# Kernel tuning notes

Hardware: AMD Instinct MI355X
Metric: run time of the kernel (lower is better)

The kernel has to match this reference:

```python
import jax, jax.numpy as jnp
import numpy as np

DIM = 256
NUM_HEADS = 4
FRAMES = 8
B_ = 32768
INNER = DIM // 2              # 128
HEAD_DIM = INNER // NUM_HEADS # 32 (actual per-head dim in forward)
SCALE = (DIM // NUM_HEADS) ** -0.5  # faithful: init uses dim//num_heads = 64


def _rel_pos_index():
    # window_size = [FRAMES, 1, 1] -> index depends only on temporal offset
    d = np.arange(FRAMES)
    idx = d[:, None] - d[None, :] + (FRAMES - 1)  # [N, N] in [0, 2F-2]
    return jnp.asarray(idx, dtype=jnp.int32)


def setup_inputs() -> dict:
    key = jax.random.key(0)
    ks = jax.random.split(key, 5)
    x = jax.random.normal(ks[0], (B_, FRAMES, DIM), dtype=jnp.float32)
    qkv_w = jax.random.normal(ks[1], (DIM, INNER * 3), dtype=jnp.float32) * 0.02
    proj_w = jax.random.normal(ks[2], (INNER, DIM), dtype=jnp.float32) * 0.02
    proj_b = jnp.zeros((DIM,), dtype=jnp.float32)
    bias_table = jax.random.normal(ks[3], (2 * FRAMES - 1, NUM_HEADS), dtype=jnp.float32) * 0.02
    rel_index = _rel_pos_index()
    return {"x": x, "qkv_w": qkv_w, "proj_w": proj_w, "proj_b": proj_b,
            "bias_table": bias_table, "rel_index": rel_index}


def reference(x, qkv_w, proj_w, proj_b, bias_table, rel_index):
    B, N, C = x.shape
    h, hd = NUM_HEADS, HEAD_DIM
    qkv = (x @ qkv_w).reshape(B, N, 3, h, hd)
    qkv = jnp.transpose(qkv, (2, 0, 3, 1, 4))  # [3, B, h, N, hd]
    q, k, v = qkv[0], qkv[1], qkv[2]
    attn = jnp.einsum('bhnd,bhmd->bhnm', q * SCALE, k)  # [B, h, N, N]
    # gather relative position bias: [N, N, h] -> [h, N, N]
    bias = bias_table[rel_index[:N, :N]]  # [N, N, h]
    attn = attn + jnp.transpose(bias, (2, 0, 1))[None]
    attn = jax.nn.softmax(attn, axis=-1)
    out = jnp.einsum('bhnm,bhmd->bhnd', attn, v)       # [B, h, N, hd]
    out = jnp.transpose(out, (0, 2, 1, 3)).reshape(B, N, h * hd)  # [B, N, 128]
    return out @ proj_w + proj_b
```

## Files before the change

### kernel.cpp

```cpp
#include <hip/hip_runtime.h>
#include <hip/hip_bf16.h>

typedef short bf16x8 __attribute__((ext_vector_type(8)));
typedef float f32x4 __attribute__((ext_vector_type(4)));

#define B_TOT    32768
#define ROWS     64

#define WSQ_ELT  0
#define WSP_ELT  98304
#define WS_BYTES 262144

#define WQ_OFF   0
#define QK_OFF   26112
#define BIAS_OFF 39424
#define PB_OFF   40704
#define OUT_OFF  0
#define LDS_BYTES 41728

__device__ __forceinline__ unsigned short f2b(float f) {
    union { float f; unsigned u; } v; v.f = f;
    unsigned r = (v.u + 0x7fffu + ((v.u >> 16) & 1u)) >> 16;
    return (unsigned short)r;
}
__device__ __forceinline__ float b2f(unsigned short u) {
    union { unsigned u; float f; } v; v.u = ((unsigned)u) << 16; return v.f;
}

__global__ __launch_bounds__(256)
void prep_w(const float* __restrict__ qkv_w, const float* __restrict__ proj_w,
            unsigned short* __restrict__ ws)
{
    __shared__ float tile[64][65];
    const int bid = blockIdx.x;
    const float* src; unsigned short* dst; int ldw, ldk, tr0, tc0;
    if (bid < 24) {
        int kr = bid / 6, cg = bid % 6;
        src = qkv_w; dst = ws + WSQ_ELT; ldw = 384; ldk = 256;
        tr0 = kr * 64; tc0 = cg * 64;
    } else {
        int b = bid - 24; int kr = b / 4, cg = b % 4;
        src = proj_w; dst = ws + WSP_ELT; ldw = 256; ldk = 128;
        tr0 = kr * 64; tc0 = cg * 64;
    }
    const int t = threadIdx.x;
    #pragma unroll
    for (int i = 0; i < 16; ++i) {
        int idx = i * 256 + t;
        int r = idx >> 6, c = idx & 63;
        tile[r][c] = src[(size_t)(tr0 + r) * ldw + tc0 + c];
    }
    __syncthreads();
    #pragma unroll
    for (int i = 0; i < 2; ++i) {
        int idx = i * 256 + t;
        int c = idx >> 3, r0 = (idx & 7) * 8;
        union { unsigned short u[8]; uint4 v; } pk;
        #pragma unroll
        for (int j = 0; j < 8; ++j) pk.u[j] = f2b(tile[r0 + j][c]);
        *(uint4*)&dst[(size_t)(tc0 + c) * ldk + tr0 + r0] = pk.v;
    }
}

__global__ __launch_bounds__(256)
void ta_fused(const float* __restrict__ x,
              const unsigned short* __restrict__ ws,
              const float* __restrict__ proj_b,
              const float* __restrict__ bias_table,
              const int* __restrict__ rel_index,
              float* __restrict__ out)
{
    __shared__ __align__(16) char smem[LDS_BYTES];
    unsigned short* wqs = (unsigned short*)(smem + WQ_OFF);
    unsigned short* qks = (unsigned short*)(smem + QK_OFF);
    float* bias_s = (float*)(smem + BIAS_OFF);
    float* pbs    = (float*)(smem + PB_OFF);
    float* outs   = (float*)(smem + OUT_OFF);

    const unsigned short* wsq = ws + WSQ_ELT;
    const unsigned short* wsp = ws + WSP_ELT;

    const int tid = threadIdx.x;
    const int l   = tid & 63;
    const int w   = tid >> 6;
    const int l15 = l & 15;
    const int l4  = l >> 4;
    const long wg = blockIdx.x;

    bf16x8 af[8];
    {
        const float* xg = x + wg * (ROWS * 256) + (size_t)(16 * w + l15) * 256;
        #pragma unroll
        for (int s = 0; s < 8; ++s) {
            f32x4 d0 = *(const f32x4*)(xg + s * 32 + l4 * 8);
            f32x4 d1 = *(const f32x4*)(xg + s * 32 + l4 * 8 + 4);
            union { unsigned short u[8]; bf16x8 v; } pk;
            #pragma unroll
            for (int j = 0; j < 4; ++j) pk.u[j] = f2b(d0[j]);
            #pragma unroll
            for (int j = 0; j < 4; ++j) pk.u[4 + j] = f2b(d1[j]);
            af[s] = pk.v;
        }
    }
    {
        int n = tid >> 5, m = (tid >> 2) & 7, hh = tid & 3;
        int ri = rel_index[n * 8 + m];
        bias_s[n * 40 + m * 5 + hh] = bias_table[ri * 4 + hh];
        pbs[tid] = proj_b[tid];
    }

    bf16x8 ofrag0, ofrag1, ofrag2, ofrag3;
    const f32x4 zero4 = {0.f, 0.f, 0.f, 0.f};

    #pragma unroll 1
    for (int h = 0; h < 4; ++h) {
        f32x4 acc[6];
        #pragma unroll
        for (int i = 0; i < 6; ++i) acc[i] = zero4;

        #pragma unroll
        for (int c = 0; c < 2; ++c) {
            __syncthreads();
            #pragma unroll
            for (int u = 0; u < 6; ++u) {
                int idx = u * 256 + tid;
                int rr = idx >> 4, seg = idx & 15;
                int p = rr >> 5, within = rr & 31;
                uint4 d = *(const uint4*)&wsq[(size_t)(p * 128 + h * 32 + within) * 256 + c * 128 + seg * 8];
                *(uint4*)&wqs[rr * 136 + seg * 8] = d;
            }
            __syncthreads();
            #pragma unroll
            for (int ks2 = 0; ks2 < 4; ++ks2) {
                bf16x8 a = af[c * 4 + ks2];
                #pragma unroll
                for (int ct = 0; ct < 6; ++ct) {
                    bf16x8 b = *(bf16x8*)&wqs[(ct * 16 + l15) * 136 + ks2 * 32 + l4 * 8];
                    acc[ct] = __builtin_amdgcn_mfma_f32_16x16x32_bf16(a, b, acc[ct], 0, 0, 0);
                }
            }
        }
        #pragma unroll
        for (int ct = 0; ct < 6; ++ct) {
            #pragma unroll
            for (int j = 0; j < 4; ++j) {
                int row = 16 * w + l4 * 4 + j;
                qks[row * 104 + ct * 16 + l15] = f2b(acc[ct][j]);
            }
        }
        __syncthreads();

        {
            const int r  = 16 * w + l15;
            const int rb = r & ~7;
            const int n  = r & 7;
            const int ds = l4;
            float qf[8];
            {
                bf16x8 qv = *(bf16x8*)&qks[r * 104 + ds * 8];
                #pragma unroll
                for (int j = 0; j < 8; ++j) qf[j] = b2f((unsigned short)qv[j]);
            }
            float sp[8];
            #pragma unroll
            for (int m = 0; m < 8; ++m) {
                bf16x8 kv = *(bf16x8*)&qks[(rb + m) * 104 + 32 + ds * 8];
                float s = 0.f;
                #pragma unroll
                for (int j = 0; j < 8; ++j) s += qf[j] * b2f((unsigned short)kv[j]);
                sp[m] = s;
            }
            #pragma unroll
            for (int m = 0; m < 8; ++m) {
                sp[m] += __shfl_xor(sp[m], 16);
                sp[m] += __shfl_xor(sp[m], 32);
            }
            float mx = -1e30f;
            #pragma unroll
            for (int m = 0; m < 8; ++m) {
                sp[m] = sp[m] * 0.125f + bias_s[n * 40 + m * 5 + h];
                mx = fmaxf(mx, sp[m]);
            }
            float sum = 0.f;
            #pragma unroll
            for (int m = 0; m < 8; ++m) { sp[m] = __expf(sp[m] - mx); sum += sp[m]; }
            float inv = 1.f / sum;
            float o[8] = {0.f,0.f,0.f,0.f,0.f,0.f,0.f,0.f};
            #pragma unroll
            for (int m = 0; m < 8; ++m) {
                bf16x8 vv = *(bf16x8*)&qks[(rb + m) * 104 + 64 + ds * 8];
                #pragma unroll
                for (int j = 0; j < 8; ++j) o[j] += sp[m] * b2f((unsigned short)vv[j]);
            }
            bf16x8 of;
            #pragma unroll
            for (int j = 0; j < 8; ++j) of[j] = (short)f2b(o[j] * inv);
            if      (h == 0) ofrag0 = of;
            else if (h == 1) ofrag1 = of;
            else if (h == 2) ofrag2 = of;
            else             ofrag3 = of;
        }
    }

    f32x4 acc2[16];
    #pragma unroll
    for (int i = 0; i < 16; ++i) acc2[i] = zero4;

    #pragma unroll
    for (int cc = 0; cc < 4; ++cc) {
        __syncthreads();
        #pragma unroll
        for (int u = 0; u < 4; ++u) {
            int idx = u * 256 + tid;
            int rr = idx >> 4, seg = idx & 15;
            uint4 d = *(const uint4*)&wsp[(size_t)(cc * 64 + rr) * 128 + seg * 8];
            *(uint4*)&wqs[rr * 136 + seg * 8] = d;
        }
        __syncthreads();
        #pragma unroll
        for (int ctl = 0; ctl < 4; ++ctl) {
            #pragma unroll
            for (int ks = 0; ks < 4; ++ks) {
                bf16x8 b = *(bf16x8*)&wqs[(ctl * 16 + l15) * 136 + ks * 32 + l4 * 8];
                bf16x8 a = (ks == 0) ? ofrag0 : (ks == 1) ? ofrag1 : (ks == 2) ? ofrag2 : ofrag3;
                acc2[cc * 4 + ctl] = __builtin_amdgcn_mfma_f32_16x16x32_bf16(a, b, acc2[cc * 4 + ctl], 0, 0, 0);
            }
        }
    }

    #pragma unroll
    for (int half = 0; half < 2; ++half) {
        __syncthreads();
        if ((w < 2) == (half == 0)) {
            #pragma unroll
            for (int cc = 0; cc < 4; ++cc)
              #pragma unroll
              for (int ctl = 0; ctl < 4; ++ctl)
                #pragma unroll
                for (int j = 0; j < 4; ++j) {
                    int row = 16 * (w & 1) + l4 * 4 + j;
                    int col = cc * 64 + ctl * 16 + l15;
                    outs[row * 260 + col] = acc2[cc * 4 + ctl][j] + pbs[col];
                }
        }
        __syncthreads();
        float* og = out + wg * (ROWS * 256) + half * (32 * 256);
        #pragma unroll
        for (int i = 0; i < 4; ++i) {
            int f0 = (i * 256 + tid) * 8;
            int row = f0 >> 8, col = f0 & 255;
            f32x4 v0 = *(f32x4*)&outs[row * 260 + col];
            f32x4 v1 = *(f32x4*)&outs[row * 260 + col + 4];
            *(f32x4*)(og + f0)     = v0;
            *(f32x4*)(og + f0 + 4) = v1;
        }
    }
}

extern "C" void kernel_launch(void* const* d_in, const int* in_sizes, int n_in,
                              void* d_out, int out_size, void* d_ws, size_t ws_size,
                              hipStream_t stream)
{
    (void)in_sizes; (void)n_in; (void)ws_size; (void)out_size;
    const float* x  = (const float*)d_in[0];
    const float* qw = (const float*)d_in[1];
    const float* pw = (const float*)d_in[2];
    const float* pb = (const float*)d_in[3];
    const float* bt = (const float*)d_in[4];
    const int*   ri = (const int*)d_in[5];
    float* o = (float*)d_out;
    unsigned short* ws = (unsigned short*)d_ws;

    hipLaunchKernelGGL(prep_w, dim3(32), dim3(256), 0, stream, qw, pw, ws);
    hipLaunchKernelGGL(ta_fused, dim3(B_TOT / 8), dim3(256), 0, stream,
                       x, ws, pb, bt, ri, o);
}
```

Baseline: 237.2 us.

## Double rows per workgroup so each wave reuses staged weight tiles across two M-tiles

```diff
diff --git a/kernel.cpp b/kernel.cpp
--- a/kernel.cpp
+++ b/kernel.cpp
@@ -4,24 +4,22 @@
 typedef short bf16x8 __attribute__((ext_vector_type(8)));
 typedef float f32x4 __attribute__((ext_vector_type(4)));
 
-#define B_TOT    32768
-#define ROWS     64
+#define B_TOT 32768
+#define ROWS  128
 
 #define WSQ_ELT  0
 #define WSP_ELT  98304
-#define WS_BYTES 262144
 
 #define WQ_OFF   0
 #define QK_OFF   26112
-#define BIAS_OFF 39424
-#define PB_OFF   40704
+#define BIAS_OFF 52736
+#define PB_OFF   54016
 #define OUT_OFF  0
-#define LDS_BYTES 41728
+#define LDS_BYTES 55040
 
 __device__ __forceinline__ unsigned short f2b(float f) {
-    union { float f; unsigned u; } v; v.f = f;
-    unsigned r = (v.u + 0x7fffu + ((v.u >> 16) & 1u)) >> 16;
-    return (unsigned short)r;
+    __hip_bfloat16 h = __float2bfloat16(f);
+    return reinterpret_cast<unsigned short&>(h);
 }
 __device__ __forceinline__ float b2f(unsigned short u) {
     union { unsigned u; float f; } v; v.u = ((unsigned)u) << 16; return v.f;
@@ -87,19 +85,23 @@
     const int l4  = l >> 4;
     const long wg = blockIdx.x;
 
-    bf16x8 af[8];
+    bf16x8 af[2][8];
     {
-        const float* xg = x + wg * (ROWS * 256) + (size_t)(16 * w + l15) * 256;
-        #pragma unroll
-        for (int s = 0; s < 8; ++s) {
-            f32x4 d0 = *(const f32x4*)(xg + s * 32 + l4 * 8);
-            f32x4 d1 = *(const f32x4*)(xg + s * 32 + l4 * 8 + 4);
-            union { unsigned short u[8]; bf16x8 v; } pk;
-            #pragma unroll
-            for (int j = 0; j < 4; ++j) pk.u[j] = f2b(d0[j]);
-            #pragma unroll
-            for (int j = 0; j < 4; ++j) pk.u[4 + j] = f2b(d1[j]);
-            af[s] = pk.v;
+        const float* xg = x + wg * (size_t)(ROWS * 256);
+        #pragma unroll
+        for (int mt = 0; mt < 2; ++mt) {
+            const float* xr = xg + (size_t)(32 * w + 16 * mt + l15) * 256;
+            #pragma unroll
+            for (int s = 0; s < 8; ++s) {
+                f32x4 d0 = *(const f32x4*)(xr + s * 32 + l4 * 8);
+                f32x4 d1 = *(const f32x4*)(xr + s * 32 + l4 * 8 + 4);
+                union { unsigned short u[8]; bf16x8 v; } pk;
+                #pragma unroll
+                for (int j = 0; j < 4; ++j) pk.u[j] = f2b(d0[j]);
+                #pragma unroll
+                for (int j = 0; j < 4; ++j) pk.u[4 + j] = f2b(d1[j]);
+                af[mt][s] = pk.v;
+            }
         }
     }
     {
@@ -109,14 +111,14 @@
         pbs[tid] = proj_b[tid];
     }
 
-    bf16x8 ofrag0, ofrag1, ofrag2, ofrag3;
+    bf16x8 of[2][4];
     const f32x4 zero4 = {0.f, 0.f, 0.f, 0.f};
 
     #pragma unroll 1
     for (int h = 0; h < 4; ++h) {
-        f32x4 acc[6];
-        #pragma unroll
-        for (int i = 0; i < 6; ++i) acc[i] = zero4;
+        f32x4 acc[6][2];
+        #pragma unroll
+        for (int i = 0; i < 6; ++i) { acc[i][0] = zero4; acc[i][1] = zero4; }
 
         #pragma unroll
         for (int c = 0; c < 2; ++c) {
@@ -132,39 +134,39 @@
             __syncthreads();
             #pragma unroll
             for (int ks2 = 0; ks2 < 4; ++ks2) {
-                bf16x8 a = af[c * 4 + ks2];
                 #pragma unroll
                 for (int ct = 0; ct < 6; ++ct) {
                     bf16x8 b = *(bf16x8*)&wqs[(ct * 16 + l15) * 136 + ks2 * 32 + l4 * 8];
-                    acc[ct] = __builtin_amdgcn_mfma_f32_16x16x32_bf16(a, b, acc[ct], 0, 0, 0);
+                    acc[ct][0] = __builtin_amdgcn_mfma_f32_16x16x32_bf16(af[0][c * 4 + ks2], b, acc[ct][0], 0, 0, 0);
+                    acc[ct][1] = __builtin_amdgcn_mfma_f32_16x16x32_bf16(af[1][c * 4 + ks2], b, acc[ct][1], 0, 0, 0);
                 }
             }
         }
         #pragma unroll
-        for (int ct = 0; ct < 6; ++ct) {
+        for (int ct = 0; ct < 6; ++ct)
+          #pragma unroll
+          for (int mt = 0; mt < 2; ++mt)
             #pragma unroll
             for (int j = 0; j < 4; ++j) {
-                int row = 16 * w + l4 * 4 + j;
-                qks[row * 104 + ct * 16 + l15] = f2b(acc[ct][j]);
-            }
-        }
-        __syncthreads();
-
-        {
-            const int r  = 16 * w + l15;
+                int row = 32 * w + 16 * mt + l4 * 4 + j;
+                qks[row * 104 + ct * 16 + l15] = f2b(acc[ct][mt][j]);
+            }
+
+        #pragma unroll
+        for (int mt = 0; mt < 2; ++mt) {
+            const int r  = 32 * w + 16 * mt + l15;
             const int rb = r & ~7;
             const int n  = r & 7;
-            const int ds = l4;
             float qf[8];
             {
-                bf16x8 qv = *(bf16x8*)&qks[r * 104 + ds * 8];
+                bf16x8 qv = *(bf16x8*)&qks[r * 104 + l4 * 8];
                 #pragma unroll
                 for (int j = 0; j < 8; ++j) qf[j] = b2f((unsigned short)qv[j]);
             }
             float sp[8];
             #pragma unroll
             for (int m = 0; m < 8; ++m) {
-                bf16x8 kv = *(bf16x8*)&qks[(rb + m) * 104 + 32 + ds * 8];
+                bf16x8 kv = *(bf16x8*)&qks[(rb + m) * 104 + 32 + l4 * 8];
                 float s = 0.f;
                 #pragma unroll
                 for (int j = 0; j < 8; ++j) s += qf[j] * b2f((unsigned short)kv[j]);
@@ -188,23 +190,25 @@
             float o[8] = {0.f,0.f,0.f,0.f,0.f,0.f,0.f,0.f};
             #pragma unroll
             for (int m = 0; m < 8; ++m) {
-                bf16x8 vv = *(bf16x8*)&qks[(rb + m) * 104 + 64 + ds * 8];
+                bf16x8 vv = *(bf16x8*)&qks[(rb + m) * 104 + 64 + l4 * 8];
                 #pragma unroll
                 for (int j = 0; j < 8; ++j) o[j] += sp[m] * b2f((unsigned short)vv[j]);
             }
-            bf16x8 of;
-            #pragma unroll
-            for (int j = 0; j < 8; ++j) of[j] = (short)f2b(o[j] * inv);
-            if      (h == 0) ofrag0 = of;
-            else if (h == 1) ofrag1 = of;
-            else if (h == 2) ofrag2 = of;
-            else             ofrag3 = of;
-        }
-    }
-
-    f32x4 acc2[16];
-    #pragma unroll
-    for (int i = 0; i < 16; ++i) acc2[i] = zero4;
+            bf16x8 ofr;
+            #pragma unroll
+            for (int j = 0; j < 8; ++j) ofr[j] = (short)f2b(o[j] * inv);
+            if      (h == 0) of[mt][0] = ofr;
+            else if (h == 1) of[mt][1] = ofr;
+            else if (h == 2) of[mt][2] = ofr;
+            else             of[mt][3] = ofr;
+        }
+    }
+
+    f32x4 acc2[4][4][2];
+    #pragma unroll
+    for (int i = 0; i < 4; ++i)
+      #pragma unroll
+      for (int j = 0; j < 4; ++j) { acc2[i][j][0] = zero4; acc2[i][j][1] = zero4; }
 
     #pragma unroll
     for (int cc = 0; cc < 4; ++cc) {
@@ -222,29 +226,31 @@
             #pragma unroll
             for (int ks = 0; ks < 4; ++ks) {
                 bf16x8 b = *(bf16x8*)&wqs[(ctl * 16 + l15) * 136 + ks * 32 + l4 * 8];
-                bf16x8 a = (ks == 0) ? ofrag0 : (ks == 1) ? ofrag1 : (ks == 2) ? ofrag2 : ofrag3;
-                acc2[cc * 4 + ctl] = __builtin_amdgcn_mfma_f32_16x16x32_bf16(a, b, acc2[cc * 4 + ctl], 0, 0, 0);
-            }
-        }
-    }
-
-    #pragma unroll
-    for (int half = 0; half < 2; ++half) {
-        __syncthreads();
-        if ((w < 2) == (half == 0)) {
+                acc2[cc][ctl][0] = __builtin_amdgcn_mfma_f32_16x16x32_bf16(of[0][ks], b, acc2[cc][ctl][0], 0, 0, 0);
+                acc2[cc][ctl][1] = __builtin_amdgcn_mfma_f32_16x16x32_bf16(of[1][ks], b, acc2[cc][ctl][1], 0, 0, 0);
+            }
+        }
+    }
+
+    #pragma unroll
+    for (int p = 0; p < 4; ++p) {
+        __syncthreads();
+        if (w == p) {
             #pragma unroll
             for (int cc = 0; cc < 4; ++cc)
               #pragma unroll
               for (int ctl = 0; ctl < 4; ++ctl)
                 #pragma unroll
-                for (int j = 0; j < 4; ++j) {
-                    int row = 16 * (w & 1) + l4 * 4 + j;
-                    int col = cc * 64 + ctl * 16 + l15;
-                    outs[row * 260 + col] = acc2[cc * 4 + ctl][j] + pbs[col];
-                }
-        }
-        __syncthreads();
-        float* og = out + wg * (ROWS * 256) + half * (32 * 256);
+                for (int mt = 0; mt < 2; ++mt)
+                  #pragma unroll
+                  for (int j = 0; j < 4; ++j) {
+                      int row = 16 * mt + l4 * 4 + j;
+                      int col = cc * 64 + ctl * 16 + l15;
+                      outs[row * 260 + col] = acc2[cc][ctl][mt][j] + pbs[col];
+                  }
+        }
+        __syncthreads();
+        float* og = out + wg * (size_t)(ROWS * 256) + p * (32 * 256);
         #pragma unroll
         for (int i = 0; i < 4; ++i) {
             int f0 = (i * 256 + tid) * 8;
@@ -272,6 +278,6 @@
     unsigned short* ws = (unsigned short*)d_ws;
 
     hipLaunchKernelGGL(prep_w, dim3(32), dim3(256), 0, stream, qw, pw, ws);
-    hipLaunchKernelGGL(ta_fused, dim3(B_TOT / 8), dim3(256), 0, stream,
+    hipLaunchKernelGGL(ta_fused, dim3(B_TOT / 16), dim3(256), 0, stream,
                        x, ws, pb, bt, ri, o);
 }
```

New measurement: 431.7 us. +82.0%, slower.
